# Kernel tuning notes

Hardware: AMD Instinct MI355X
Metric: run time of the kernel (lower is better)

## Reference

```python
import jax, jax.numpy as jnp
import numpy as np

T, K, E, H, I = 2048, 8, 32, 1024, 768


def setup_inputs() -> dict:
    key = jax.random.key(0)
    k0, k1, k2, k3, k4, k5 = jax.random.split(key, 6)
    sh = 1.0 / np.sqrt(H).astype(np.float32)
    si = 1.0 / np.sqrt(I).astype(np.float32)
    return {
        "hidden_states": jax.random.normal(k0, (T, H), jnp.float32),
        "top_k_index": jax.random.randint(k1, (T, K), 0, E),
        "top_k_weights": jax.random.uniform(k2, (T, K), jnp.float32),
        "gate_proj": jax.random.normal(k3, (E, I, H), jnp.float32) * sh,
        "up_proj": jax.random.normal(k4, (E, I, H), jnp.float32) * sh,
        "down_proj": jax.random.normal(k5, (E, H, I), jnp.float32) * si,
    }


def reference(hidden_states, top_k_index, top_k_weights, gate_proj, up_proj, down_proj):
    # Tokens not routed to expert e get combine weight 0, so summing the
    # weighted per-expert outputs over all experts reproduces the original
    # gather -> SwiGLU MLP -> scale -> index_add_ exactly (duplicated expert
    # hits within a token's top-k sum, matching repeated index_add_).
    n_tok = hidden_states.shape[0]
    n_exp = gate_proj.shape[0]
    combine = jnp.zeros((n_tok, n_exp), hidden_states.dtype)
    combine = combine.at[jnp.arange(n_tok)[:, None], top_k_index].add(top_k_weights)

    def body(acc, xs):
        g_w, u_w, d_w, w_e = xs  # g_w,u_w: [I,H]; d_w: [H,I]; w_e: [T]
        h = jax.nn.silu(hidden_states @ g_w.T) * (hidden_states @ u_w.T)  # [T,I]
        y = h @ d_w.T  # [T,H]
        return acc + y * w_e[:, None], None

    out, _ = jax.lax.scan(
        body,
        jnp.zeros_like(hidden_states),
        (gate_proj, up_proj, down_proj, combine.T),
    )
    return out
```

## Files before the change

kernel.cpp:

```cpp
#include <hip/hip_runtime.h>

#define T_TOK 2048
#define TOPK  8
#define NEXP  32
#define HDIM  1024
#define IDIM  768
#define NPAIR (T_TOK * TOPK)
#define BM 128
#define BK 32
#define MT_MAX (NPAIR / BM + NEXP)

typedef __attribute__((ext_vector_type(8))) short short8;
typedef __attribute__((ext_vector_type(4))) float f32x4;

__device__ __forceinline__ unsigned short f2bf(float f) {
    unsigned x = __float_as_uint(f);
    unsigned r = x + 0x7fffu + ((x >> 16) & 1u);
    return (unsigned short)(r >> 16);
}
__device__ __forceinline__ float bf2f(unsigned short u) {
    return __uint_as_float(((unsigned)u) << 16);
}

__device__ __forceinline__ void gl_lds16(const unsigned short* g, void* l) {
    __builtin_amdgcn_global_load_lds((const __attribute__((address_space(1))) void*)g,
                                     (__attribute__((address_space(3))) void*)l, 16, 0, 0);
}

__global__ void k_conv2(const float* __restrict__ src0, const float* __restrict__ src1,
                        unsigned short* __restrict__ dst, int n4each) {
    int i = blockIdx.x * 256 + threadIdx.x;
    const float* s = (i < n4each) ? src0 : src1;
    int j = (i < n4each) ? i : i - n4each;
    if (i < 2 * n4each) {
        float4 v = ((const float4*)s)[j];
        ushort4 o;
        o.x = f2bf(v.x); o.y = f2bf(v.y); o.z = f2bf(v.z); o.w = f2bf(v.w);
        ((ushort4*)dst)[i] = o;
    }
}

__global__ void k_conv(const float* __restrict__ src, unsigned short* __restrict__ dst, int n4) {
    int i = blockIdx.x * 256 + threadIdx.x;
    if (i < n4) {
        float4 v = ((const float4*)src)[i];
        ushort4 o;
        o.x = f2bf(v.x); o.y = f2bf(v.y); o.z = f2bf(v.z); o.w = f2bf(v.w);
        ((ushort4*)dst)[i] = o;
    }
}

__global__ void k_init(int* counts) {
    if (threadIdx.x < NEXP) counts[threadIdx.x] = 0;
}

__global__ void k_hist(const int* __restrict__ idx, int* __restrict__ counts) {
    int p = blockIdx.x * 256 + threadIdx.x;
    atomicAdd(&counts[idx[p]], 1);
}

__global__ void k_scan(const int* __restrict__ counts, int* __restrict__ offsets,
                       int* __restrict__ mtb, int* __restrict__ cursor) {
    if (threadIdx.x == 0) {
        int tot = 0, mt = 0;
        for (int e = 0; e < NEXP; ++e) {
            offsets[e] = tot; mtb[e] = mt;
            tot += counts[e];
            mt += (counts[e] + BM - 1) / BM;
        }
        offsets[NEXP] = tot; mtb[NEXP] = mt;
    }
    if (threadIdx.x < NEXP) cursor[threadIdx.x] = 0;
}

__global__ void k_scatter(const int* __restrict__ idx, int* __restrict__ cursor,
                          const int* __restrict__ offsets, int* __restrict__ pair_token,
                          int* __restrict__ pair_slot) {
    int p = blockIdx.x * 256 + threadIdx.x;
    int e = idx[p];
    int pos = atomicAdd(&cursor[e], 1);
    int slot = offsets[e] + pos;
    pair_token[slot] = p >> 3;
    pair_slot[p] = slot;
}

__global__ __launch_bounds__(256, 2) void k_gateup(
    const unsigned short* __restrict__ hid_bf, const unsigned short* __restrict__ gate_bf,
    const unsigned short* __restrict__ up_bf, const int* __restrict__ pair_token,
    const int* __restrict__ offsets, const int* __restrict__ mtb,
    unsigned short* __restrict__ h_mid)
{
    __shared__ short8 sA[512], sBg[512], sBu[512];
    __shared__ int sInfo[4];
    int tid = threadIdx.x;
    if (tid == 0) {
        int mt = blockIdx.x;
        if (mt >= mtb[NEXP]) { sInfo[0] = -1; }
        else {
            int e = 0;
            while (mtb[e + 1] <= mt) e++;
            sInfo[0] = e; sInfo[1] = offsets[e];
            sInfo[2] = offsets[e + 1] - offsets[e];
            sInfo[3] = (mt - mtb[e]) * BM;
        }
    }
    __syncthreads();
    int e = sInfo[0];
    if (e < 0) return;
    int off = sInfo[1], Me = sInfo[2], mrow0 = sInfo[3];
    int n0 = blockIdx.y * 128;

    int wave = tid >> 6, lane = tid & 63, quad = lane >> 4, l16 = lane & 15;

    int m0 = wave * 32 + l16, m1 = m0 + 16;
    int rp0 = mrow0 + m0, rp1 = mrow0 + m1;
    int tok0 = (rp0 < Me) ? pair_token[off + rp0] : 0;
    int tok1 = (rp1 < Me) ? pair_token[off + rp1] : 0;
    const unsigned short* aG0 = hid_bf + (size_t)tok0 * HDIM + quad * 8;
    const unsigned short* aG1 = hid_bf + (size_t)tok1 * HDIM + quad * 8;
    const unsigned short* gG0 = gate_bf + ((size_t)e * IDIM + n0 + m0) * HDIM + quad * 8;
    const unsigned short* gG1 = gate_bf + ((size_t)e * IDIM + n0 + m1) * HDIM + quad * 8;
    const unsigned short* uG0 = up_bf + ((size_t)e * IDIM + n0 + m0) * HDIM + quad * 8;
    const unsigned short* uG1 = up_bf + ((size_t)e * IDIM + n0 + m1) * HDIM + quad * 8;
    void* ldsA0 = (void*)&sA[wave * 128];  void* ldsA1 = (void*)&sA[wave * 128 + 64];
    void* ldsG0 = (void*)&sBg[wave * 128]; void* ldsG1 = (void*)&sBg[wave * 128 + 64];
    void* ldsU0 = (void*)&sBu[wave * 128]; void* ldsU1 = (void*)&sBu[wave * 128 + 64];

    int wm = (wave & 1) * 64, wn = (wave >> 1) * 64;
    int aBase = (wm >> 4) * 64 + quad * 16 + l16;
    int bBase = (wn >> 4) * 64 + quad * 16 + l16;

    f32x4 zero = {0.f, 0.f, 0.f, 0.f};
    f32x4 accg[4][4], accu[4][4];
#pragma unroll
    for (int i = 0; i < 4; ++i)
#pragma unroll
        for (int j = 0; j < 4; ++j) { accg[i][j] = zero; accu[i][j] = zero; }

    for (int k0 = 0; k0 < HDIM; k0 += BK) {
        gl_lds16(aG0 + k0, ldsA0); gl_lds16(aG1 + k0, ldsA1);
        gl_lds16(gG0 + k0, ldsG0); gl_lds16(gG1 + k0, ldsG1);
        gl_lds16(uG0 + k0, ldsU0); gl_lds16(uG1 + k0, ldsU1);
        __syncthreads();
        short8 af[4];
#pragma unroll
        for (int fm = 0; fm < 4; ++fm) af[fm] = sA[aBase + fm * 64];
#pragma unroll
        for (int fn = 0; fn < 4; ++fn) {
            short8 bg = sBg[bBase + fn * 64];
            short8 bu = sBu[bBase + fn * 64];
#pragma unroll
            for (int fm = 0; fm < 4; ++fm) {
                accg[fm][fn] = __builtin_amdgcn_mfma_f32_16x16x32_bf16(af[fm], bg, accg[fm][fn], 0, 0, 0);
                accu[fm][fn] = __builtin_amdgcn_mfma_f32_16x16x32_bf16(af[fm], bu, accu[fm][fn], 0, 0, 0);
            }
        }
        __syncthreads();
    }

#pragma unroll
    for (int fm = 0; fm < 4; ++fm)
#pragma unroll
        for (int fn = 0; fn < 4; ++fn)
#pragma unroll
            for (int r = 0; r < 4; ++r) {
                int mloc = wm + fm * 16 + quad * 4 + r;
                int prow = mrow0 + mloc;
                if (prow < Me) {
                    int col = n0 + wn + fn * 16 + l16;
                    float g = accg[fm][fn][r], u = accu[fm][fn][r];
                    float h = g / (1.f + __expf(-g)) * u;
                    h_mid[(size_t)(off + prow) * IDIM + col] = f2bf(h);
                }
            }
}

__global__ __launch_bounds__(256, 2) void k_down(
    const unsigned short* __restrict__ h_mid, const unsigned short* __restrict__ down_bf,
    const int* __restrict__ offsets, const int* __restrict__ mtb,
    unsigned short* __restrict__ y_pair)
{
    __shared__ short8 sA[512], sB[1024];
    __shared__ int sInfo[4];
    int tid = threadIdx.x;
    if (tid == 0) {
        int mt = blockIdx.x;
        if (mt >= mtb[NEXP]) { sInfo[0] = -1; }
        else {
            int e = 0;
            while (mtb[e + 1] <= mt) e++;
            sInfo[0] = e; sInfo[1] = offsets[e];
            sInfo[2] = offsets[e + 1] - offsets[e];
            sInfo[3] = (mt - mtb[e]) * BM;
        }
    }
    __syncthreads();
    int e = sInfo[0];
    if (e < 0) return;
    int off = sInfo[1], Me = sInfo[2], mrow0 = sInfo[3];
    int n0 = blockIdx.y * 256;

    int wave = tid >> 6, lane = tid & 63, quad = lane >> 4, l16 = lane & 15;

    int m0 = wave * 32 + l16, m1 = m0 + 16;
    int rp0 = mrow0 + m0; if (rp0 >= Me) rp0 = 0;
    int rp1 = mrow0 + m1; if (rp1 >= Me) rp1 = 0;
    const unsigned short* aG0 = h_mid + (size_t)(off + rp0) * IDIM + quad * 8;
    const unsigned short* aG1 = h_mid + (size_t)(off + rp1) * IDIM + quad * 8;
    const unsigned short* bG0 = down_bf + ((size_t)e * HDIM + n0 + wave * 64 + l16) * IDIM + quad * 8;
    const unsigned short* bG1 = bG0 + (size_t)16 * IDIM;
    const unsigned short* bG2 = bG0 + (size_t)32 * IDIM;
    const unsigned short* bG3 = bG0 + (size_t)48 * IDIM;
    void* ldsA0 = (void*)&sA[wave * 128];      void* ldsA1 = (void*)&sA[wave * 128 + 64];
    void* ldsB0 = (void*)&sB[wave * 256];      void* ldsB1 = (void*)&sB[wave * 256 + 64];
    void* ldsB2 = (void*)&sB[wave * 256 + 128]; void* ldsB3 = (void*)&sB[wave * 256 + 192];

    int wm = (wave & 1) * 64, wn = (wave >> 1) * 128;
    int aBase = (wm >> 4) * 64 + quad * 16 + l16;
    int bBase = (wn >> 4) * 64 + quad * 16 + l16;

    f32x4 zero = {0.f, 0.f, 0.f, 0.f};
    f32x4 acc[4][8];
#pragma unroll
    for (int i = 0; i < 4; ++i)
#pragma unroll
        for (int j = 0; j < 8; ++j) acc[i][j] = zero;

    for (int k0 = 0; k0 < IDIM; k0 += BK) {
        gl_lds16(aG0 + k0, ldsA0); gl_lds16(aG1 + k0, ldsA1);
        gl_lds16(bG0 + k0, ldsB0); gl_lds16(bG1 + k0, ldsB1);
        gl_lds16(bG2 + k0, ldsB2); gl_lds16(bG3 + k0, ldsB3);
        __syncthreads();
        short8 af[4];
#pragma unroll
        for (int fm = 0; fm < 4; ++fm) af[fm] = sA[aBase + fm * 64];
#pragma unroll
        for (int fn = 0; fn < 8; ++fn) {
            short8 bf = sB[bBase + fn * 64];
#pragma unroll
            for (int fm = 0; fm < 4; ++fm)
                acc[fm][fn] = __builtin_amdgcn_mfma_f32_16x16x32_bf16(af[fm], bf, acc[fm][fn], 0, 0, 0);
        }
        __syncthreads();
    }

#pragma unroll
    for (int fm = 0; fm < 4; ++fm)
#pragma unroll
        for (int fn = 0; fn < 8; ++fn)
#pragma unroll
            for (int r = 0; r < 4; ++r) {
                int mloc = wm + fm * 16 + quad * 4 + r;
                int prow = mrow0 + mloc;
                if (prow < Me) {
                    int col = n0 + wn + fn * 16 + l16;
                    y_pair[(size_t)(off + prow) * HDIM + col] = f2bf(acc[fm][fn][r]);
                }
            }
}

__global__ void k_reduce(const unsigned short* __restrict__ y_pair,
                         const int* __restrict__ pair_slot,
                         const float* __restrict__ topw, float* __restrict__ out)
{
    int t = blockIdx.x;
    __shared__ int ss[TOPK];
    __shared__ float sw[TOPK];
    if (threadIdx.x < TOPK) {
        ss[threadIdx.x] = pair_slot[t * TOPK + threadIdx.x];
        sw[threadIdx.x] = topw[t * TOPK + threadIdx.x];
    }
    __syncthreads();
    int c = threadIdx.x * 4;
    float a0 = 0.f, a1 = 0.f, a2 = 0.f, a3 = 0.f;
    for (int k = 0; k < TOPK; ++k) {
        const unsigned short* yr = y_pair + (size_t)ss[k] * HDIM + c;
        uint2 v = *(const uint2*)yr;
        float w = sw[k];
        a0 += w * bf2f((unsigned short)(v.x & 0xffff));
        a1 += w * bf2f((unsigned short)(v.x >> 16));
        a2 += w * bf2f((unsigned short)(v.y & 0xffff));
        a3 += w * bf2f((unsigned short)(v.y >> 16));
    }
    float4 o = {a0, a1, a2, a3};
    *(float4*)(out + (size_t)t * HDIM + c) = o;
}

extern "C" void kernel_launch(void* const* d_in, const int* in_sizes, int n_in,
                              void* d_out, int out_size, void* d_ws, size_t ws_size,
                              hipStream_t stream) {
    (void)in_sizes; (void)n_in; (void)out_size; (void)ws_size;
    const float* hidden = (const float*)d_in[0];
    const int*   tki    = (const int*)d_in[1];
    const float* tkw    = (const float*)d_in[2];
    const float* gate   = (const float*)d_in[3];
    const float* up     = (const float*)d_in[4];
    const float* down   = (const float*)d_in[5];
    float* out = (float*)d_out;

    char* w = (char*)d_ws;
    unsigned short* h_mid   = (unsigned short*)w;
    unsigned short* hid_bf  = (unsigned short*)(w + 25165824);
    unsigned short* gate_bf = (unsigned short*)(w + 29360128);
    unsigned short* up_bf   = (unsigned short*)(w + 79691776);
    unsigned short* down_bf = gate_bf;
    unsigned short* y_pair  = up_bf;
    int* ib = (int*)(w + 130023424);
    int* pair_token = ib;
    int* pair_slot  = ib + NPAIR;
    int* counts     = ib + 2 * NPAIR;
    int* cursor     = counts + NEXP;
    int* offsets    = cursor + NEXP;
    int* mtb        = offsets + NEXP + 1;

    const int W4 = NEXP * IDIM * HDIM / 4;
    const int H4 = T_TOK * HDIM / 4;

    k_init<<<1, 64, 0, stream>>>(counts);
    k_hist<<<NPAIR / 256, 256, 0, stream>>>(tki, counts);
    k_scan<<<1, 64, 0, stream>>>(counts, offsets, mtb, cursor);
    k_scatter<<<NPAIR / 256, 256, 0, stream>>>(tki, cursor, offsets, pair_token, pair_slot);

    k_conv<<<(H4 + 255) / 256, 256, 0, stream>>>(hidden, hid_bf, H4);
    k_conv2<<<(2 * W4 + 255) / 256, 256, 0, stream>>>(gate, up, gate_bf, W4);

    k_gateup<<<dim3(MT_MAX, IDIM / 128), 256, 0, stream>>>(hid_bf, gate_bf, up_bf,
                                                           pair_token, offsets, mtb, h_mid);

    k_conv<<<(W4 + 255) / 256, 256, 0, stream>>>(down, down_bf, W4);

    k_down<<<dim3(MT_MAX, HDIM / 256), 256, 0, stream>>>(h_mid, down_bf, offsets, mtb, y_pair);
    k_reduce<<<T_TOK, 256, 0, stream>>>(y_pair, pair_slot, tkw, out);
}
```

Measured before the change: 557.6 us.

## Double-buffer LDS tiles in MoE GEMMs with prefetch overlap and tile swizzle

Both grouped GEMM kernels now use two LDS buffers. The next K-tile is loaded asynchronously with global_load_lds while MFMAs run on the current one, and a single barrier per step replaces the two per iteration. The expert lookup per M-tile becomes a parallel search across 32 threads instead of a serial loop, and block indices are swizzled so neighbouring tiles interleave for better cache sharing. LDS use doubles, which could lower occupancy, and the mt swizzle assumes the grid is a multiple of 16.

```diff
diff --git a/kernel.cpp b/kernel.cpp
--- a/kernel.cpp
+++ b/kernel.cpp
@@ -26,6 +26,16 @@
     __builtin_amdgcn_global_load_lds((const __attribute__((address_space(1))) void*)g,
                                      (__attribute__((address_space(3))) void*)l, 16, 0, 0);
 }
+
+__device__ __forceinline__ int mt_swz(int bx) {
+    return ((bx >> 4) << 4) | ((bx & 7) << 1) | ((bx >> 3) & 1);
+}
+
+#define WSYNC do { \
+    asm volatile("s_waitcnt vmcnt(0)" ::: "memory"); \
+    __builtin_amdgcn_s_barrier(); \
+    __builtin_amdgcn_sched_barrier(0); \
+} while (0)
 
 __global__ void k_conv2(const float* __restrict__ src0, const float* __restrict__ src1,
                         unsigned short* __restrict__ dst, int n4each) {
@@ -90,18 +100,17 @@
     const int* __restrict__ offsets, const int* __restrict__ mtb,
     unsigned short* __restrict__ h_mid)
 {
-    __shared__ short8 sA[512], sBg[512], sBu[512];
+    __shared__ short8 sBuf[2][1536];
     __shared__ int sInfo[4];
     int tid = threadIdx.x;
-    if (tid == 0) {
-        int mt = blockIdx.x;
-        if (mt >= mtb[NEXP]) { sInfo[0] = -1; }
-        else {
-            int e = 0;
-            while (mtb[e + 1] <= mt) e++;
-            sInfo[0] = e; sInfo[1] = offsets[e];
-            sInfo[2] = offsets[e + 1] - offsets[e];
-            sInfo[3] = (mt - mtb[e]) * BM;
+    int mt = mt_swz(blockIdx.x);
+    if (tid == 0 && mt >= mtb[NEXP]) sInfo[0] = -1;
+    if (tid < NEXP) {
+        int lo = mtb[tid], hi = mtb[tid + 1];
+        if (lo <= mt && mt < hi) {
+            sInfo[0] = tid; sInfo[1] = offsets[tid];
+            sInfo[2] = offsets[tid + 1] - offsets[tid];
+            sInfo[3] = (mt - lo) * BM;
         }
     }
     __syncthreads();
@@ -122,9 +131,9 @@
     const unsigned short* gG1 = gate_bf + ((size_t)e * IDIM + n0 + m1) * HDIM + quad * 8;
     const unsigned short* uG0 = up_bf + ((size_t)e * IDIM + n0 + m0) * HDIM + quad * 8;
     const unsigned short* uG1 = up_bf + ((size_t)e * IDIM + n0 + m1) * HDIM + quad * 8;
-    void* ldsA0 = (void*)&sA[wave * 128];  void* ldsA1 = (void*)&sA[wave * 128 + 64];
-    void* ldsG0 = (void*)&sBg[wave * 128]; void* ldsG1 = (void*)&sBg[wave * 128 + 64];
-    void* ldsU0 = (void*)&sBu[wave * 128]; void* ldsU1 = (void*)&sBu[wave * 128 + 64];
+    const int dA = wave * 128;
+    const int dG = 512 + wave * 128;
+    const int dU = 1024 + wave * 128;
 
     int wm = (wave & 1) * 64, wn = (wave >> 1) * 64;
     int aBase = (wm >> 4) * 64 + quad * 16 + l16;
@@ -137,25 +146,37 @@
 #pragma unroll
         for (int j = 0; j < 4; ++j) { accg[i][j] = zero; accu[i][j] = zero; }
 
-    for (int k0 = 0; k0 < HDIM; k0 += BK) {
-        gl_lds16(aG0 + k0, ldsA0); gl_lds16(aG1 + k0, ldsA1);
-        gl_lds16(gG0 + k0, ldsG0); gl_lds16(gG1 + k0, ldsG1);
-        gl_lds16(uG0 + k0, ldsU0); gl_lds16(uG1 + k0, ldsU1);
-        __syncthreads();
-        short8 af[4];
-#pragma unroll
-        for (int fm = 0; fm < 4; ++fm) af[fm] = sA[aBase + fm * 64];
-#pragma unroll
-        for (int fn = 0; fn < 4; ++fn) {
-            short8 bg = sBg[bBase + fn * 64];
-            short8 bu = sBu[bBase + fn * 64];
-#pragma unroll
-            for (int fm = 0; fm < 4; ++fm) {
-                accg[fm][fn] = __builtin_amdgcn_mfma_f32_16x16x32_bf16(af[fm], bg, accg[fm][fn], 0, 0, 0);
-                accu[fm][fn] = __builtin_amdgcn_mfma_f32_16x16x32_bf16(af[fm], bu, accu[fm][fn], 0, 0, 0);
-            }
-        }
-        __syncthreads();
+#define STAGE_GU(b, k0) do { \
+        short8* nb_ = &sBuf[b][0]; \
+        gl_lds16(aG0 + (k0), (void*)(nb_ + dA));      gl_lds16(aG1 + (k0), (void*)(nb_ + dA + 64)); \
+        gl_lds16(gG0 + (k0), (void*)(nb_ + dG));      gl_lds16(gG1 + (k0), (void*)(nb_ + dG + 64)); \
+        gl_lds16(uG0 + (k0), (void*)(nb_ + dU));      gl_lds16(uG1 + (k0), (void*)(nb_ + dU + 64)); \
+    } while (0)
+
+#define COMP_GU(b) do { \
+        const short8* cb_ = &sBuf[b][0]; \
+        short8 af_[4]; \
+        _Pragma("unroll") for (int fm = 0; fm < 4; ++fm) af_[fm] = cb_[aBase + fm * 64]; \
+        _Pragma("unroll") for (int fn = 0; fn < 4; ++fn) { \
+            short8 bg_ = cb_[512 + bBase + fn * 64]; \
+            short8 bu_ = cb_[1024 + bBase + fn * 64]; \
+            _Pragma("unroll") for (int fm = 0; fm < 4; ++fm) { \
+                accg[fm][fn] = __builtin_amdgcn_mfma_f32_16x16x32_bf16(af_[fm], bg_, accg[fm][fn], 0, 0, 0); \
+                accu[fm][fn] = __builtin_amdgcn_mfma_f32_16x16x32_bf16(af_[fm], bu_, accu[fm][fn], 0, 0, 0); \
+            } \
+        } \
+    } while (0)
+
+    STAGE_GU(0, 0);
+    WSYNC;
+#pragma unroll 1
+    for (int it = 0; it < HDIM / BK; it += 2) {
+        STAGE_GU(1, (it + 1) * BK);
+        COMP_GU(0);
+        WSYNC;
+        if (it + 2 < HDIM / BK) STAGE_GU(0, (it + 2) * BK);
+        COMP_GU(1);
+        WSYNC;
     }
 
 #pragma unroll
@@ -180,18 +201,17 @@
     const int* __restrict__ offsets, const int* __restrict__ mtb,
     unsigned short* __restrict__ y_pair)
 {
-    __shared__ short8 sA[512], sB[1024];
+    __shared__ short8 sBuf[2][1536];
     __shared__ int sInfo[4];
     int tid = threadIdx.x;
-    if (tid == 0) {
-        int mt = blockIdx.x;
-        if (mt >= mtb[NEXP]) { sInfo[0] = -1; }
-        else {
-            int e = 0;
-            while (mtb[e + 1] <= mt) e++;
-            sInfo[0] = e; sInfo[1] = offsets[e];
-            sInfo[2] = offsets[e + 1] - offsets[e];
-            sInfo[3] = (mt - mtb[e]) * BM;
+    int mt = mt_swz(blockIdx.x);
+    if (tid == 0 && mt >= mtb[NEXP]) sInfo[0] = -1;
+    if (tid < NEXP) {
+        int lo = mtb[tid], hi = mtb[tid + 1];
+        if (lo <= mt && mt < hi) {
+            sInfo[0] = tid; sInfo[1] = offsets[tid];
+            sInfo[2] = offsets[tid + 1] - offsets[tid];
+            sInfo[3] = (mt - lo) * BM;
         }
     }
     __syncthreads();
@@ -211,9 +231,8 @@
     const unsigned short* bG1 = bG0 + (size_t)16 * IDIM;
     const unsigned short* bG2 = bG0 + (size_t)32 * IDIM;
     const unsigned short* bG3 = bG0 + (size_t)48 * IDIM;
-    void* ldsA0 = (void*)&sA[wave * 128];      void* ldsA1 = (void*)&sA[wave * 128 + 64];
-    void* ldsB0 = (void*)&sB[wave * 256];      void* ldsB1 = (void*)&sB[wave * 256 + 64];
-    void* ldsB2 = (void*)&sB[wave * 256 + 128]; void* ldsB3 = (void*)&sB[wave * 256 + 192];
+    const int dA = wave * 128;
+    const int dB = 512 + wave * 256;
 
     int wm = (wave & 1) * 64, wn = (wave >> 1) * 128;
     int aBase = (wm >> 4) * 64 + quad * 16 + l16;
@@ -226,22 +245,34 @@
 #pragma unroll
         for (int j = 0; j < 8; ++j) acc[i][j] = zero;
 
-    for (int k0 = 0; k0 < IDIM; k0 += BK) {
-        gl_lds16(aG0 + k0, ldsA0); gl_lds16(aG1 + k0, ldsA1);
-        gl_lds16(bG0 + k0, ldsB0); gl_lds16(bG1 + k0, ldsB1);
-        gl_lds16(bG2 + k0, ldsB2); gl_lds16(bG3 + k0, ldsB3);
-        __syncthreads();
-        short8 af[4];
-#pragma unroll
-        for (int fm = 0; fm < 4; ++fm) af[fm] = sA[aBase + fm * 64];
-#pragma unroll
-        for (int fn = 0; fn < 8; ++fn) {
-            short8 bf = sB[bBase + fn * 64];
-#pragma unroll
-            for (int fm = 0; fm < 4; ++fm)
-                acc[fm][fn] = __builtin_amdgcn_mfma_f32_16x16x32_bf16(af[fm], bf, acc[fm][fn], 0, 0, 0);
-        }
-        __syncthreads();
+#define STAGE_DN(b, k0) do { \
+        short8* nb_ = &sBuf[b][0]; \
+        gl_lds16(aG0 + (k0), (void*)(nb_ + dA));       gl_lds16(aG1 + (k0), (void*)(nb_ + dA + 64)); \
+        gl_lds16(bG0 + (k0), (void*)(nb_ + dB));       gl_lds16(bG1 + (k0), (void*)(nb_ + dB + 64)); \
+        gl_lds16(bG2 + (k0), (void*)(nb_ + dB + 128)); gl_lds16(bG3 + (k0), (void*)(nb_ + dB + 192)); \
+    } while (0)
+
+#define COMP_DN(b) do { \
+        const short8* cb_ = &sBuf[b][0]; \
+        short8 af_[4]; \
+        _Pragma("unroll") for (int fm = 0; fm < 4; ++fm) af_[fm] = cb_[aBase + fm * 64]; \
+        _Pragma("unroll") for (int fn = 0; fn < 8; ++fn) { \
+            short8 bb_ = cb_[512 + bBase + fn * 64]; \
+            _Pragma("unroll") for (int fm = 0; fm < 4; ++fm) \
+                acc[fm][fn] = __builtin_amdgcn_mfma_f32_16x16x32_bf16(af_[fm], bb_, acc[fm][fn], 0, 0, 0); \
+        } \
+    } while (0)
+
+    STAGE_DN(0, 0);
+    WSYNC;
+#pragma unroll 1
+    for (int it = 0; it < IDIM / BK; it += 2) {
+        STAGE_DN(1, (it + 1) * BK);
+        COMP_DN(0);
+        WSYNC;
+        if (it + 2 < IDIM / BK) STAGE_DN(0, (it + 2) * BK);
+        COMP_DN(1);
+        WSYNC;
     }
 
 #pragma unroll
```

Measured after the change: 560.8 us. No clear change (+0.6%).
